# Performance work log

Measured on AMD Instinct MI355X. Metric: run time of the kernel, lower is better.

Reference implementation:

```python
import jax, jax.numpy as jnp
import numpy as np

# dims: S sets, M max items, DIN input feat, DM model dim (= head_size), H heads, L layers
S, M, DIN, DM, H, DH, L = 48, 128, 128, 128, 4, 128, 2
ALPHA = 0.3  # tf.keras.layers.LeakyReLU default alpha


def gelu(x):
    return jax.nn.gelu(x, approximate=False)  # tf.nn.gelu default is exact


def leaky(x):
    return jnp.where(x >= 0, x, ALPHA * x)


def set_norm(x, size):
    # masked per-set normalization over all items*features; pad rows (feature-sum == 0) are zeroed
    d = x.shape[-1]
    mask = (jnp.sum(x, axis=-1, keepdims=True) != 0).astype(x.dtype)  # [S,M,1]
    denom = size * d  # [S]
    mean = jnp.sum(x, axis=(1, 2)) / denom
    diff = x - mean[:, None, None]
    var = jnp.sum(jnp.square(diff) * mask, axis=(1, 2)) / denom
    return diff / (jnp.sqrt(var)[:, None, None] + 1e-8) * mask


def masked_softmax(s):
    # original masks by *nonzero score values*, not an additive bias
    mask = s != 0
    e = jnp.where(mask, jnp.exp(s - jnp.max(s, axis=-1, keepdims=True)), 0.0)
    return e / (jnp.sum(e, axis=-1, keepdims=True) + 1e-10)


def attention(x, wq, wk, wv, wh):
    split = lambda z: z.reshape(z.shape[0], z.shape[1], H, DH).transpose(0, 2, 1, 3)  # [S,H,M,D]
    q, k, v = split(x @ wq), split(x @ wk), split(x @ wv)
    s = jnp.einsum('shmd,shnd->shmn', q, k) / np.float32(np.sqrt(DH))
    a = masked_softmax(s)
    o = jnp.einsum('shmn,shnd->shmd', a, v).transpose(0, 2, 1, 3).reshape(x.shape[0], x.shape[1], H * DH)
    return o @ wh


def forward(x, size, W_proj, Wq, Wk, Wv, Wh, Wfc, Wc, w2):
    mask = (jnp.sum(x != 0, axis=-1, keepdims=True) > 0).astype(x.dtype)  # [S,M,1] valid-item mask
    h = gelu(x @ W_proj) * mask
    for l in range(L):
        a = attention(h, Wq[l], Wk[l], Wv[l], Wh[l]) * mask
        h = set_norm(h + a, size)
        f = gelu(h @ Wfc[l]) * mask
        h = set_norm(h + f, size)
    # cross_set_score (tuple branch, x == y): pairwise per-head set scores
    z = (h @ Wc).reshape(h.shape[0], h.shape[1], H, DH).transpose(0, 2, 1, 3)  # [S,H,M,D]
    s = leaky(jnp.einsum('jhmd,ihnd->jihmn', z, z) / np.float32(np.sqrt(DH)))  # [Sy,Sx,H,My,Mx]
    scores = jnp.sum(s, axis=(-1, -2)) / size[None, :, None] / np.float32(M)  # [Sy,Sx,H]
    return scores @ w2  # [Sy,Sx,1]


def setup_inputs() -> dict:
    key = jax.random.key(0)
    ks = jax.random.split(key, 10)
    x = jax.random.normal(ks[0], (S, M, DIN), jnp.float32)
    x_size = jax.random.randint(ks[1], (S,), 1, M + 1, jnp.int32)
    x = x * (jnp.arange(M)[None, :] < x_size[:, None])[:, :, None]  # zero-pad beyond set size
    sc = lambda n: np.float32(1.0 / np.sqrt(n))
    W_proj = jax.random.normal(ks[2], (DIN, DM), jnp.float32) * sc(DIN)
    Wq = jax.random.normal(ks[3], (L, DM, H * DH), jnp.float32) * sc(DM)
    Wk = jax.random.normal(ks[4], (L, DM, H * DH), jnp.float32) * sc(DM)
    Wv = jax.random.normal(ks[5], (L, DM, H * DH), jnp.float32) * sc(DM)
    Wh = jax.random.normal(ks[6], (L, H * DH, DM), jnp.float32) * sc(H * DH)
    Wfc = jax.random.normal(ks[7], (L, DM, DM), jnp.float32) * sc(DM)
    Wc = jax.random.normal(ks[8], (DM, H * DH), jnp.float32) * sc(DM)
    w2 = jax.random.normal(ks[9], (H, 1), jnp.float32) * sc(H)
    return dict(x=x, x_size=x_size, W_proj=W_proj, Wq=Wq, Wk=Wk, Wv=Wv, Wh=Wh, Wfc=Wfc, Wc=Wc, w2=w2)


def reference(x, x_size, W_proj, Wq, Wk, Wv, Wh, Wfc, Wc, w2):
    size = jnp.maximum(x_size, 1).astype(jnp.float32)
    return forward(x, size, W_proj, Wq, Wk, Wv, Wh, Wfc, Wc, w2)
```

## Files before the change

kernel.cpp:

```cpp
#include <hip/hip_runtime.h>
#include <hip/hip_bf16.h>
#include <math.h>

typedef unsigned short u16;
typedef short bf16x8 __attribute__((ext_vector_type(8)));
typedef float f32x4 __attribute__((ext_vector_type(4)));
typedef float f32x16 __attribute__((ext_vector_type(16)));

__device__ __forceinline__ u16 f2b(float f){
  union { float f; unsigned u; } c; c.f = f;
  unsigned u = c.u;
  unsigned r = (u + 0x7fffu + ((u >> 16) & 1u)) >> 16;
  return (u16)r;
}
__device__ __forceinline__ u16 f2bh(float f){
  union { __bf16 b; u16 u; } c; c.b = (__bf16)f; return c.u;
}
__device__ __forceinline__ unsigned pack2(float a, float b){
  return (unsigned)f2bh(a) | ((unsigned)f2bh(b) << 16);
}
__device__ __forceinline__ float gelu_f(float x){
  return 0.5f * x * (1.0f + erff(x * 0.70710678118654752f));
}

__global__ __launch_bounds__(256) void prep_weights(
    const float* __restrict__ Wproj, const float* __restrict__ Wq,
    const float* __restrict__ Wk,    const float* __restrict__ Wv,
    const float* __restrict__ Whp,   const float* __restrict__ Wfc,
    const float* __restrict__ Wc,    u16* __restrict__ wT,
    float* __restrict__ out)
{
  __shared__ __align__(16) u16 Ah[128*136];
  __shared__ __align__(16) u16 Bv[128*136];
  int bid = blockIdx.x, tid = threadIdx.x;
  if (bid >= 320) {
    int o = (bid - 320) * 256 + tid;
    if (o < 2304) out[o] = 0.0f;
    return;
  }
  if (bid < 312) {
    int cid = bid * 256 + tid;
    if (cid >= 34816 && cid < 67584) return;
    int region, lh = 0, c;
    if      (cid < 2048)  { region = 0; c = cid; }
    else if (cid < 18432) { int o = cid - 2048;  region = 1; lh = o >> 11; c = o & 2047; }
    else if (cid < 34816) { int o = cid - 18432; region = 2; lh = o >> 11; c = o & 2047; }
    else if (cid < 71680) { int o = cid - 67584; region = 5; lh = o >> 11; c = o & 2047; }
    else                  { int o = cid - 71680; region = 6; lh = o >> 11; c = o & 2047; }
    int l16 = c & 15, quad = (c >> 4) & 3, ks = (c >> 6) & 3, nt = c >> 8;
    int n = nt * 16 + l16, kb = ks * 32 + quad * 8;
    int l = lh >> 2, hh = lh & 3;
    const float rs = 0.08838834764831845f;
    u16 tmp[8];
#pragma unroll
    for (int e = 0; e < 8; ++e) {
      int k = kb + e;
      float v;
      switch (region) {
        case 0: v = Wproj[k * 128 + n]; break;
        case 1: v = Wq[l * 65536 + k * 512 + hh * 128 + n] * rs; break;
        case 2: v = Wk[l * 65536 + k * 512 + hh * 128 + n]; break;
        case 5: v = Wfc[lh * 16384 + k * 128 + n]; break;
        default: v = Wc[k * 512 + lh * 128 + n]; break;
      }
      tmp[e] = f2b(v);
    }
    *(uint4*)(wT + (size_t)cid * 8) = *(uint4*)tmp;
    return;
  }
  int lhb = bid - 312; int l = lhb >> 2, hh = lhb & 3;
#pragma unroll
  for (int it = 0; it < 64; ++it) {
    int idx = it * 256 + tid;
    int a = idx & 127, b = idx >> 7;
    Ah[a * 136 + b] = f2b(Whp[l * 65536 + (hh * 128 + b) * 128 + a]);
    Bv[b * 136 + a] = f2b(Wv[l * 65536 + b * 512 + hh * 128 + a]);
  }
  __syncthreads();
  int wv = tid >> 6, lane = tid & 63, quad = lane >> 4, l16 = lane & 15;
  f32x4 acc[2][8] = {};
  for (int ks = 0; ks < 4; ++ks) {
    bf16x8 aF[2], bF[8];
#pragma unroll
    for (int i = 0; i < 2; ++i)
      aF[i] = *(const bf16x8*)(Ah + ((wv*2+i)*16 + l16)*136 + ks*32 + quad*8);
#pragma unroll
    for (int n = 0; n < 8; ++n)
      bF[n] = *(const bf16x8*)(Bv + (n*16 + l16)*136 + ks*32 + quad*8);
#pragma unroll
    for (int i = 0; i < 2; ++i)
#pragma unroll
      for (int n = 0; n < 8; ++n)
        acc[i][n] = __builtin_amdgcn_mfma_f32_16x16x32_bf16(aF[i], bF[n], acc[i][n], 0, 0, 0);
  }
  size_t base = 278528 + (size_t)lhb * 16384;
#pragma unroll
  for (int i = 0; i < 2; ++i)
#pragma unroll
    for (int n2 = 0; n2 < 8; ++n2)
#pragma unroll
      for (int g = 0; g < 4; ++g) {
        int n = (wv*2+i)*16 + quad*4 + g;
        int k = n2*16 + l16;
        wT[base + (size_t)((((n>>4)*4 + (k>>5))*4 + ((k>>3)&3))*16 + (n&15))*8 + (k&7)]
            = f2b(acc[i][n2][g]);
      }
}

__device__ __forceinline__ void gemm_g(const u16* A, const u16* __restrict__ Bg,
    f32x4 (*acc)[4], int wr, int wc, int quad, int l16, int lane){
#pragma unroll
  for (int ks = 0; ks < 4; ++ks){
    bf16x8 aF[2], bF[4];
#pragma unroll
    for (int i = 0; i < 2; ++i)
      aF[i] = *(const bf16x8*)(A + ((wr*2+i)*16 + l16)*136 + ks*32 + quad*8);
#pragma unroll
    for (int n = 0; n < 4; ++n)
      bF[n] = *(const bf16x8*)(Bg + ((size_t)(((wc*4+n)*4 + ks)*64 + lane))*8);
#pragma unroll
    for (int i = 0; i < 2; ++i)
#pragma unroll
      for (int n = 0; n < 4; ++n)
        acc[i][n] = __builtin_amdgcn_mfma_f32_16x16x32_bf16(aF[i], bF[n], acc[i][n], 0, 0, 0);
  }
}

__device__ __forceinline__ void write_rm(u16* dst, f32x4 (*acc)[4],
                                         int wr, int wc, int quad, int l16){
#pragma unroll
  for (int i = 0; i < 2; ++i)
#pragma unroll
    for (int n = 0; n < 4; ++n)
#pragma unroll
      for (int g = 0; g < 4; ++g)
        dst[((wr*2+i)*16 + quad*4 + g)*136 + (wc*4+n)*16 + l16] = f2bh(acc[i][n][g]);
}

__device__ __forceinline__ void write_tr(u16* dst, f32x4 (*acc)[4],
                                         int wr, int wc, int quad, int l16){
#pragma unroll
  for (int i = 0; i < 2; ++i)
#pragma unroll
    for (int n = 0; n < 4; ++n)
#pragma unroll
      for (int g = 0; g < 4; ++g)
        dst[((wc*4+n)*16 + l16)*136 + (wr*2+i)*16 + quad*4 + g] = f2bh(acc[i][n][g]);
}

__device__ __forceinline__ void block_reduce2(float &s1, float &s2,
                                              float* red, int wv, int lane){
#pragma unroll
  for (int off = 1; off < 64; off <<= 1){
    s1 += __shfl_xor(s1, off, 64);
    s2 += __shfl_xor(s2, off, 64);
  }
  if (lane == 0){ red[wv*2] = s1; red[wv*2+1] = s2; }
  __syncthreads();
  s1 = red[0]+red[2]+red[4]+red[6]+red[8]+red[10]+red[12]+red[14];
  s2 = red[1]+red[3]+red[5]+red[7]+red[9]+red[11]+red[13]+red[15];
  __syncthreads();
}

__global__ __launch_bounds__(512, 2) void trunk(
    const float* __restrict__ x, const int* __restrict__ xsize,
    const u16* __restrict__ wT, u16* __restrict__ zg)
{
  __shared__ __align__(16) u16 hA[128*136];
  __shared__ __align__(16) u16 qP[128*136];
  __shared__ __align__(16) u16 kB[128*136];
  __shared__ __align__(16) u16 vB[128*136];
  __shared__ float svalid[128];
  __shared__ float red[16];
  int tid = threadIdx.x;
  int wv = tid >> 6, lane = tid & 63, quad = lane >> 4, l16 = lane & 15;
  int wr = wv >> 1, wc = wv & 1;
  int s = blockIdx.x;
  int sz = xsize[s]; if (sz < 1) sz = 1;
  int Mt = (sz + 15) >> 4, Mk = (sz + 31) >> 5;
  float den = (float)sz * 128.0f;

#pragma unroll
  for (int it = 0; it < 4; ++it) {
    int ch = tid + it * 512; int r = ch >> 4, cc = ch & 15;
    const float* p = x + ((size_t)s * 128 + r) * 128 + cc * 8;
    float4 u0 = *(const float4*)p, u1 = *(const float4*)(p + 4);
    int nz = (u0.x!=0.f)|(u0.y!=0.f)|(u0.z!=0.f)|(u0.w!=0.f)|
             (u1.x!=0.f)|(u1.y!=0.f)|(u1.z!=0.f)|(u1.w!=0.f);
    nz |= __shfl_xor(nz,1,64); nz |= __shfl_xor(nz,2,64);
    nz |= __shfl_xor(nz,4,64); nz |= __shfl_xor(nz,8,64);
    if ((tid & 15) == 0) svalid[r] = nz ? 1.f : 0.f;
    uint4 w;
    w.x = pack2(u0.x,u0.y); w.y = pack2(u0.z,u0.w);
    w.z = pack2(u1.x,u1.y); w.w = pack2(u1.z,u1.w);
    *(uint4*)(hA + r*136 + cc*8) = w;
  }
  __syncthreads();

  f32x4 hR[2][4];
  {
    f32x4 acc[2][4] = {};
    gemm_g(hA, wT, acc, wr, wc, quad, l16, lane);
    __syncthreads();
#pragma unroll
    for (int i = 0; i < 2; ++i)
#pragma unroll
      for (int n = 0; n < 4; ++n)
#pragma unroll
        for (int g = 0; g < 4; ++g) {
          int row = (wr*2+i)*16 + quad*4 + g;
          float gg = gelu_f(acc[i][n][g]) * svalid[row];
          hR[i][n][g] = gg;
          hA[row*136 + (wc*4+n)*16 + l16] = f2bh(gg);
        }
    __syncthreads();
  }

#pragma unroll 1
  for (int l = 0; l < 2; ++l) {
    f32x4 aR[2][4] = {};
#pragma unroll 1
    for (int hh = 0; hh < 4; ++hh) {
      int lh = l * 4 + hh;
      {
        f32x4 qa[2][4] = {};
        gemm_g(hA, wT + 16384 + lh*16384, qa, wr, wc, quad, l16, lane);
        write_rm(qP, qa, wr, wc, quad, l16);
      }
      {
        f32x4 ka[2][4] = {};
        gemm_g(hA, wT + 147456 + lh*16384, ka, wr, wc, quad, l16, lane);
        write_rm(kB, ka, wr, wc, quad, l16);
      }
      {
        f32x4 va[2][4] = {};
        gemm_g(hA, wT + 278528 + lh*16384, va, wr, wc, quad, l16, lane);
        write_tr(vB, va, wr, wc, quad, l16);
      }
      __syncthreads();
      if (wv < Mt) {
        bf16x8 qA[4];
#pragma unroll
        for (int ks = 0; ks < 4; ++ks)
          qA[ks] = *(const bf16x8*)(qP + (wv*16 + l16)*136 + ks*32 + quad*8);
        f32x4 sacc[8] = {};
#pragma unroll
        for (int ks = 0; ks < 4; ++ks) {
          bf16x8 bF[8];
#pragma unroll
          for (int j = 0; j < 8; ++j)
            if (j < Mt) bF[j] = *(const bf16x8*)(kB + (j*16+l16)*136 + ks*32 + quad*8);
#pragma unroll
          for (int j = 0; j < 8; ++j)
            if (j < Mt) sacc[j] = __builtin_amdgcn_mfma_f32_16x16x32_bf16(qA[ks], bF[j], sacc[j], 0, 0, 0);
        }
        for (int g = 0; g < 4; ++g) {
          float vals[8]; float rmax = -1e30f;
#pragma unroll
          for (int j = 0; j < 8; ++j)
            if (j < Mt) {
              float v = sacc[j][g];
              vals[j] = v;
              rmax = fmaxf(rmax, v);
            }
          for (int off = 1; off < 16; off <<= 1) rmax = fmaxf(rmax, __shfl_xor(rmax, off, 64));
          if (sz < 128) rmax = fmaxf(rmax, 0.0f);
          float rsum = 0.f;
#pragma unroll
          for (int j = 0; j < 8; ++j)
            if (j < Mt) {
              float e = (vals[j] != 0.0f) ? __expf(vals[j] - rmax) : 0.0f;
              vals[j] = e; rsum += e;
            }
          for (int off = 1; off < 16; off <<= 1) rsum += __shfl_xor(rsum, off, 64);
          float inv = 1.0f / (rsum + 1e-10f);
#pragma unroll
          for (int j = 0; j < 8; ++j)
            if (j < Mt) sacc[j][g] = vals[j] * inv;
        }
#pragma unroll
        for (int j = 0; j < 8; ++j)
          if (j < Mt)
#pragma unroll
            for (int g = 0; g < 4; ++g)
              qP[(wv*16 + quad*4 + g)*136 + j*16 + l16] = f2bh(sacc[j][g]);
      }
      __syncthreads();
#pragma unroll
      for (int i = 0; i < 2; ++i) {
        int mtile = wr*2 + i;
        if (mtile < Mt) {
          for (int ks = 0; ks < Mk; ++ks) {
            bf16x8 aF = *(const bf16x8*)(qP + (mtile*16 + l16)*136 + ks*32 + quad*8);
            bf16x8 bF[4];
#pragma unroll
            for (int n = 0; n < 4; ++n)
              bF[n] = *(const bf16x8*)(vB + ((wc*4+n)*16+l16)*136 + ks*32 + quad*8);
#pragma unroll
            for (int n = 0; n < 4; ++n)
              aR[i][n] = __builtin_amdgcn_mfma_f32_16x16x32_bf16(aF, bF[n], aR[i][n], 0, 0, 0);
          }
        }
      }
      __syncthreads();
    }

    {
      float ls1 = 0.f, ls2 = 0.f;
#pragma unroll
      for (int i = 0; i < 2; ++i)
#pragma unroll
        for (int n = 0; n < 4; ++n)
#pragma unroll
          for (int g = 0; g < 4; ++g) {
            int row = (wr*2+i)*16 + quad*4 + g;
            float u = hR[i][n][g] + aR[i][n][g] * svalid[row];
            hR[i][n][g] = u;
            ls1 += u; ls2 += u * u;
          }
      block_reduce2(ls1, ls2, red, wv, lane);
      float mean = ls1 / den;
      float var = ls2 / den - mean * mean; if (var < 0.f) var = 0.f;
      float inv = 1.0f / (sqrtf(var) + 1e-8f);
#pragma unroll
      for (int i = 0; i < 2; ++i)
#pragma unroll
        for (int n = 0; n < 4; ++n)
#pragma unroll
          for (int g = 0; g < 4; ++g) {
            int row = (wr*2+i)*16 + quad*4 + g;
            float hn = (hR[i][n][g] - mean) * inv * svalid[row];
            hR[i][n][g] = hn;
            hA[row*136 + (wc*4+n)*16 + l16] = f2bh(hn);
          }
      __syncthreads();
    }
    {
      f32x4 fa[2][4] = {};
      gemm_g(hA, wT + 540672 + l*16384, fa, wr, wc, quad, l16, lane);
      float ls1 = 0.f, ls2 = 0.f;
#pragma unroll
      for (int i = 0; i < 2; ++i)
#pragma unroll
        for (int n = 0; n < 4; ++n)
#pragma unroll
          for (int g = 0; g < 4; ++g) {
            int row = (wr*2+i)*16 + quad*4 + g;
            float u = hR[i][n][g] + gelu_f(fa[i][n][g]) * svalid[row];
            hR[i][n][g] = u;
            ls1 += u; ls2 += u * u;
          }
      block_reduce2(ls1, ls2, red, wv, lane);
      float mean = ls1 / den;
      float var = ls2 / den - mean * mean; if (var < 0.f) var = 0.f;
      float inv = 1.0f / (sqrtf(var) + 1e-8f);
#pragma unroll
      for (int i = 0; i < 2; ++i)
#pragma unroll
        for (int n = 0; n < 4; ++n)
#pragma unroll
          for (int g = 0; g < 4; ++g) {
            int row = (wr*2+i)*16 + quad*4 + g;
            float hn = (hR[i][n][g] - mean) * inv * svalid[row];
            hR[i][n][g] = hn;
            hA[row*136 + (wc*4+n)*16 + l16] = f2bh(hn);
          }
      __syncthreads();
    }
  }

#pragma unroll 1
  for (int hh = 0; hh < 4; ++hh) {
    f32x4 za[2][4] = {};
    gemm_g(hA, wT + 573440 + hh*16384, za, wr, wc, quad, l16, lane);
    u16* zb = zg + (((size_t)s*4 + hh) << 14);
#pragma unroll
    for (int i = 0; i < 2; ++i)
#pragma unroll
      for (int n = 0; n < 4; ++n)
#pragma unroll
        for (int g = 0; g < 4; ++g) {
          int row = (wr*2+i)*16 + quad*4 + g;
          int col = (wc*4+n)*16 + l16;
          zb[(size_t)(((row>>5)*8 + (col>>4))*512 + ((col>>3)&1)*256
                      + (row&31)*8 + (col&7))] = f2bh(za[i][n][g]);
        }
  }
}

__global__ __launch_bounds__(256) void cross_kernel(
    const u16* __restrict__ zg, const float* __restrict__ w2,
    float* __restrict__ out, const int* __restrict__ xsize)
{
  __shared__ float red[4];
  int tid = threadIdx.x, wave = tid >> 6, lane = tid & 63;
  int t4 = blockIdx.x;
  int pr = t4 >> 2, hh = t4 & 3;
  float jf = (97.0f - sqrtf(9409.0f - 8.0f * (float)pr)) * 0.5f;
  int j = (int)jf; if (j > 47) j = 47; if (j < 0) j = 0;
  while (j > 0 && j * 48 - (j * (j - 1)) / 2 > pr) --j;
  while ((j + 1) * 48 - ((j + 1) * j) / 2 <= pr) ++j;
  int i = j + pr - (j * 48 - (j * (j - 1)) / 2);
  int sj = xsize[j]; if (sj < 1) sj = 1;
  int si = xsize[i]; if (si < 1) si = 1;
  int MjT = (sj + 31) >> 5, MiT = (si + 31) >> 5;
  const u16* zj = zg + (((size_t)j * 4 + hh) << 14);
  const u16* zi = zg + (((size_t)i * 4 + hh) << 14);
  int gA = (wave >> 1) * 2, gB = (wave & 1) * 2;
  bool a0 = gA < MjT, a1 = (gA + 1) < MjT;
  bool b0 = gB < MiT, b1 = (gB + 1) < MiT;
  f32x16 acc[2][2] = {};
  if ((a0 || a1) && (b0 || b1)) {
#pragma unroll
    for (int ks = 0; ks < 8; ++ks) {
      bf16x8 aF[2], bF[2];
      if (a0) aF[0] = *(const bf16x8*)(zj + (size_t)((gA    )*8 + ks)*512 + lane*8);
      if (a1) aF[1] = *(const bf16x8*)(zj + (size_t)((gA + 1)*8 + ks)*512 + lane*8);
      if (b0) bF[0] = *(const bf16x8*)(zi + (size_t)((gB    )*8 + ks)*512 + lane*8);
      if (b1) bF[1] = *(const bf16x8*)(zi + (size_t)((gB + 1)*8 + ks)*512 + lane*8);
      if (a0 && b0) acc[0][0] = __builtin_amdgcn_mfma_f32_32x32x16_bf16(aF[0], bF[0], acc[0][0], 0, 0, 0);
      if (a0 && b1) acc[0][1] = __builtin_amdgcn_mfma_f32_32x32x16_bf16(aF[0], bF[1], acc[0][1], 0, 0, 0);
      if (a1 && b0) acc[1][0] = __builtin_amdgcn_mfma_f32_32x32x16_bf16(aF[1], bF[0], acc[1][0], 0, 0, 0);
      if (a1 && b1) acc[1][1] = __builtin_amdgcn_mfma_f32_32x32x16_bf16(aF[1], bF[1], acc[1][1], 0, 0, 0);
    }
  }
  float s1 = 0.f, s2 = 0.f;
#pragma unroll
  for (int ii = 0; ii < 2; ++ii)
#pragma unroll
    for (int jj = 0; jj < 2; ++jj) {
      bool tact = (ii ? a1 : a0) && (jj ? b1 : b0);
      if (tact)
#pragma unroll
        for (int r = 0; r < 16; ++r) {
          float a = acc[ii][jj][r];
          s1 += a; s2 += fabsf(a);
        }
    }
  const float rs = 0.08838834764831845f;
  float tp = rs * (0.65f * s1 + 0.35f * s2);
  for (int off = 1; off < 64; off <<= 1) tp += __shfl_xor(tp, off, 64);
  if (lane == 0) red[wave] = tp;
  __syncthreads();
  if (tid == 0) {
    float T = red[0] + red[1] + red[2] + red[3];
    float w = w2[hh];
    atomicAdd(out + j * 48 + i, T * w / ((float)si * 128.0f));
    if (i != j)
      atomicAdd(out + i * 48 + j, T * w / ((float)sj * 128.0f));
  }
}

extern "C" void kernel_launch(void* const* d_in, const int* in_sizes, int n_in,
                              void* d_out, int out_size, void* d_ws, size_t ws_size,
                              hipStream_t stream)
{
  const float* x     = (const float*)d_in[0];
  const int*   xsize = (const int*)d_in[1];
  const float* Wproj = (const float*)d_in[2];
  const float* Wq    = (const float*)d_in[3];
  const float* Wk    = (const float*)d_in[4];
  const float* Wv    = (const float*)d_in[5];
  const float* Whp   = (const float*)d_in[6];
  const float* Wfc   = (const float*)d_in[7];
  const float* Wc    = (const float*)d_in[8];
  const float* w2    = (const float*)d_in[9];
  float* out = (float*)d_out;

  char* ws = (char*)d_ws;
  size_t off = 0;
  auto alloc = [&](size_t bytes) -> char* {
    char* p = ws + off;
    off += (bytes + 255) & ~(size_t)255;
    return p;
  };
  u16* wT = (u16*)alloc(638976 * 2);
  u16* zg = (u16*)alloc((size_t)3145728 * 2);

  prep_weights<<<329, 256, 0, stream>>>(Wproj, Wq, Wk, Wv, Whp, Wfc, Wc, wT, out);
  trunk<<<48, 512, 0, stream>>>(x, xsize, wT, zg);
  cross_kernel<<<4704, 256, 0, stream>>>(zg, w2, out, xsize);
}
```

Baseline: 224.5 us.

## Fuse trunk and cross-score kernels into one cooperative persistent kernel with flags

The separate trunk and cross_kernel launches are merged into a single cooperative kernel of 256 blocks. The first 48 blocks run the per-set trunk, write z, and publish a per-set ready flag with release semantics. All blocks then pull pairwise cross-score work items from an atomic counter, two items per block, and spin on the flags of the two sets they need. This is meant to remove a kernel launch boundary and let cross-score work overlap the tail of the trunk, at the cost of spin-waiting, atomics and one more flag-reset block in prep_weights.

```diff
diff --git a/kernel.cpp b/kernel.cpp
--- a/kernel.cpp
+++ b/kernel.cpp
@@ -28,11 +28,12 @@
     const float* __restrict__ Wk,    const float* __restrict__ Wv,
     const float* __restrict__ Whp,   const float* __restrict__ Wfc,
     const float* __restrict__ Wc,    u16* __restrict__ wT,
-    float* __restrict__ out)
+    float* __restrict__ out, int* __restrict__ flags)
 {
   __shared__ __align__(16) u16 Ah[128*136];
   __shared__ __align__(16) u16 Bv[128*136];
   int bid = blockIdx.x, tid = threadIdx.x;
+  if (bid == 329) { if (tid < 64) flags[tid] = 0; return; }
   if (bid >= 320) {
     int o = (bid - 320) * 256 + tid;
     if (o < 2304) out[o] = 0.0f;
@@ -162,9 +163,11 @@
   __syncthreads();
 }
 
-__global__ __launch_bounds__(512, 2) void trunk(
+__global__ __launch_bounds__(512, 2) void mega(
     const float* __restrict__ x, const int* __restrict__ xsize,
-    const u16* __restrict__ wT, u16* __restrict__ zg)
+    const u16* __restrict__ wT, u16* __restrict__ zg,
+    const float* __restrict__ w2, float* __restrict__ out,
+    int* __restrict__ flags)
 {
   __shared__ __align__(16) u16 hA[128*136];
   __shared__ __align__(16) u16 qP[128*136];
@@ -172,141 +175,215 @@
   __shared__ __align__(16) u16 vB[128*136];
   __shared__ float svalid[128];
   __shared__ float red[16];
+  __shared__ int s_item;
+  __shared__ float redx[8];
   int tid = threadIdx.x;
-  int wv = tid >> 6, lane = tid & 63, quad = lane >> 4, l16 = lane & 15;
-  int wr = wv >> 1, wc = wv & 1;
-  int s = blockIdx.x;
-  int sz = xsize[s]; if (sz < 1) sz = 1;
-  int Mt = (sz + 15) >> 4, Mk = (sz + 31) >> 5;
-  float den = (float)sz * 128.0f;
-
-#pragma unroll
-  for (int it = 0; it < 4; ++it) {
-    int ch = tid + it * 512; int r = ch >> 4, cc = ch & 15;
-    const float* p = x + ((size_t)s * 128 + r) * 128 + cc * 8;
-    float4 u0 = *(const float4*)p, u1 = *(const float4*)(p + 4);
-    int nz = (u0.x!=0.f)|(u0.y!=0.f)|(u0.z!=0.f)|(u0.w!=0.f)|
-             (u1.x!=0.f)|(u1.y!=0.f)|(u1.z!=0.f)|(u1.w!=0.f);
-    nz |= __shfl_xor(nz,1,64); nz |= __shfl_xor(nz,2,64);
-    nz |= __shfl_xor(nz,4,64); nz |= __shfl_xor(nz,8,64);
-    if ((tid & 15) == 0) svalid[r] = nz ? 1.f : 0.f;
-    uint4 w;
-    w.x = pack2(u0.x,u0.y); w.y = pack2(u0.z,u0.w);
-    w.z = pack2(u1.x,u1.y); w.w = pack2(u1.z,u1.w);
-    *(uint4*)(hA + r*136 + cc*8) = w;
-  }
-  __syncthreads();
-
-  f32x4 hR[2][4];
-  {
-    f32x4 acc[2][4] = {};
-    gemm_g(hA, wT, acc, wr, wc, quad, l16, lane);
+  int bid = blockIdx.x;
+  int* counter = flags + 48;
+  const float rs = 0.08838834764831845f;
+
+  if (bid < 48) {
+    int wv = tid >> 6, lane = tid & 63, quad = lane >> 4, l16 = lane & 15;
+    int wr = wv >> 1, wc = wv & 1;
+    int s = bid;
+    int sz = xsize[s]; if (sz < 1) sz = 1;
+    int Mt = (sz + 15) >> 4, Mk = (sz + 31) >> 5;
+    float den = (float)sz * 128.0f;
+
+#pragma unroll
+    for (int it = 0; it < 4; ++it) {
+      int ch = tid + it * 512; int r = ch >> 4, cc = ch & 15;
+      const float* p = x + ((size_t)s * 128 + r) * 128 + cc * 8;
+      float4 u0 = *(const float4*)p, u1 = *(const float4*)(p + 4);
+      int nz = (u0.x!=0.f)|(u0.y!=0.f)|(u0.z!=0.f)|(u0.w!=0.f)|
+               (u1.x!=0.f)|(u1.y!=0.f)|(u1.z!=0.f)|(u1.w!=0.f);
+      nz |= __shfl_xor(nz,1,64); nz |= __shfl_xor(nz,2,64);
+      nz |= __shfl_xor(nz,4,64); nz |= __shfl_xor(nz,8,64);
+      if ((tid & 15) == 0) svalid[r] = nz ? 1.f : 0.f;
+      uint4 w;
+      w.x = pack2(u0.x,u0.y); w.y = pack2(u0.z,u0.w);
+      w.z = pack2(u1.x,u1.y); w.w = pack2(u1.z,u1.w);
+      *(uint4*)(hA + r*136 + cc*8) = w;
+    }
     __syncthreads();
-#pragma unroll
-    for (int i = 0; i < 2; ++i)
-#pragma unroll
-      for (int n = 0; n < 4; ++n)
-#pragma unroll
-        for (int g = 0; g < 4; ++g) {
-          int row = (wr*2+i)*16 + quad*4 + g;
-          float gg = gelu_f(acc[i][n][g]) * svalid[row];
-          hR[i][n][g] = gg;
-          hA[row*136 + (wc*4+n)*16 + l16] = f2bh(gg);
-        }
-    __syncthreads();
-  }
+
+    f32x4 hR[2][4];
+    {
+      f32x4 acc[2][4] = {};
+      gemm_g(hA, wT, acc, wr, wc, quad, l16, lane);
+      __syncthreads();
+#pragma unroll
+      for (int i = 0; i < 2; ++i)
+#pragma unroll
+        for (int n = 0; n < 4; ++n)
+#pragma unroll
+          for (int g = 0; g < 4; ++g) {
+            int row = (wr*2+i)*16 + quad*4 + g;
+            float gg = gelu_f(acc[i][n][g]) * svalid[row];
+            hR[i][n][g] = gg;
+            hA[row*136 + (wc*4+n)*16 + l16] = f2bh(gg);
+          }
+      __syncthreads();
+    }
 
 #pragma unroll 1
-  for (int l = 0; l < 2; ++l) {
-    f32x4 aR[2][4] = {};
+    for (int l = 0; l < 2; ++l) {
+      f32x4 aR[2][4] = {};
+#pragma unroll 1
+      for (int hh = 0; hh < 4; ++hh) {
+        int lh = l * 4 + hh;
+        {
+          f32x4 qa[2][4] = {};
+          gemm_g(hA, wT + 16384 + lh*16384, qa, wr, wc, quad, l16, lane);
+          write_rm(qP, qa, wr, wc, quad, l16);
+        }
+        {
+          f32x4 ka[2][4] = {};
+          gemm_g(hA, wT + 147456 + lh*16384, ka, wr, wc, quad, l16, lane);
+          write_rm(kB, ka, wr, wc, quad, l16);
+        }
+        {
+          f32x4 va[2][4] = {};
+          gemm_g(hA, wT + 278528 + lh*16384, va, wr, wc, quad, l16, lane);
+          write_tr(vB, va, wr, wc, quad, l16);
+        }
+        __syncthreads();
+        if (wv < Mt) {
+          bf16x8 qA[4];
+#pragma unroll
+          for (int ks = 0; ks < 4; ++ks)
+            qA[ks] = *(const bf16x8*)(qP + (wv*16 + l16)*136 + ks*32 + quad*8);
+          f32x4 sacc[8] = {};
+#pragma unroll
+          for (int ks = 0; ks < 4; ++ks) {
+            bf16x8 bF[8];
+#pragma unroll
+            for (int j = 0; j < 8; ++j)
+              if (j < Mt) bF[j] = *(const bf16x8*)(kB + (j*16+l16)*136 + ks*32 + quad*8);
+#pragma unroll
+            for (int j = 0; j < 8; ++j)
+              if (j < Mt) sacc[j] = __builtin_amdgcn_mfma_f32_16x16x32_bf16(qA[ks], bF[j], sacc[j], 0, 0, 0);
+          }
+          for (int g = 0; g < 4; ++g) {
+            float vals[8]; float rmax = -1e30f;
+#pragma unroll
+            for (int j = 0; j < 8; ++j)
+              if (j < Mt) {
+                float v = sacc[j][g];
+                vals[j] = v;
+                rmax = fmaxf(rmax, v);
+              }
+            for (int off = 1; off < 16; off <<= 1) rmax = fmaxf(rmax, __shfl_xor(rmax, off, 64));
+            if (sz < 128) rmax = fmaxf(rmax, 0.0f);
+            float rsum = 0.f;
+#pragma unroll
+            for (int j = 0; j < 8; ++j)
+              if (j < Mt) {
+                float e = (vals[j] != 0.0f) ? __expf(vals[j] - rmax) : 0.0f;
+                vals[j] = e; rsum += e;
+              }
+            for (int off = 1; off < 16; off <<= 1) rsum += __shfl_xor(rsum, off, 64);
+            float inv = 1.0f / (rsum + 1e-10f);
+#pragma unroll
+            for (int j = 0; j < 8; ++j)
+              if (j < Mt) sacc[j][g] = vals[j] * inv;
+          }
+#pragma unroll
+          for (int j = 0; j < 8; ++j)
+            if (j < Mt)
+#pragma unroll
+              for (int g = 0; g < 4; ++g)
+                qP[(wv*16 + quad*4 + g)*136 + j*16 + l16] = f2bh(sacc[j][g]);
+        }
+        __syncthreads();
+#pragma unroll
+        for (int i = 0; i < 2; ++i) {
+          int mtile = wr*2 + i;
+          if (mtile < Mt) {
+            for (int ks = 0; ks < Mk; ++ks) {
+              bf16x8 aF = *(const bf16x8*)(qP + (mtile*16 + l16)*136 + ks*32 + quad*8);
+              bf16x8 bF[4];
+#pragma unroll
+              for (int n = 0; n < 4; ++n)
+                bF[n] = *(const bf16x8*)(vB + ((wc*4+n)*16+l16)*136 + ks*32 + quad*8);
+#pragma unroll
+              for (int n = 0; n < 4; ++n)
+                aR[i][n] = __builtin_amdgcn_mfma_f32_16x16x32_bf16(aF, bF[n], aR[i][n], 0, 0, 0);
+            }
+          }
+        }
+        __syncthreads();
+      }
+
+      {
+        float ls1 = 0.f, ls2 = 0.f;
+#pragma unroll
+        for (int i = 0; i < 2; ++i)
+#pragma unroll
+          for (int n = 0; n < 4; ++n)
+#pragma unroll
+            for (int g = 0; g < 4; ++g) {
+              int row = (wr*2+i)*16 + quad*4 + g;
+              float u = hR[i][n][g] + aR[i][n][g] * svalid[row];
+              hR[i][n][g] = u;
+              ls1 += u; ls2 += u * u;
+            }
+        block_reduce2(ls1, ls2, red, wv, lane);
+        float mean = ls1 / den;
+        float var = ls2 / den - mean * mean; if (var < 0.f) var = 0.f;
+        float inv = 1.0f / (sqrtf(var) + 1e-8f);
+#pragma unroll
+        for (int i = 0; i < 2; ++i)
+#pragma unroll
+          for (int n = 0; n < 4; ++n)
+#pragma unroll
+            for (int g = 0; g < 4; ++g) {
+              int row = (wr*2+i)*16 + quad*4 + g;
+              float hn = (hR[i][n][g] - mean) * inv * svalid[row];
+              hR[i][n][g] = hn;
+              hA[row*136 + (wc*4+n)*16 + l16] = f2bh(hn);
+            }
+        __syncthreads();
+      }
+      {
+        f32x4 fa[2][4] = {};
+        gemm_g(hA, wT + 540672 + l*16384, fa, wr, wc, quad, l16, lane);
+        float ls1 = 0.f, ls2 = 0.f;
+#pragma unroll
+        for (int i = 0; i < 2; ++i)
+#pragma unroll
+          for (int n = 0; n < 4; ++n)
+#pragma unroll
+            for (int g = 0; g < 4; ++g) {
+              int row = (wr*2+i)*16 + quad*4 + g;
+              float u = hR[i][n][g] + gelu_f(fa[i][n][g]) * svalid[row];
+              hR[i][n][g] = u;
+              ls1 += u; ls2 += u * u;
+            }
+        block_reduce2(ls1, ls2, red, wv, lane);
+        float mean = ls1 / den;
+        float var = ls2 / den - mean * mean; if (var < 0.f) var = 0.f;
+        float inv = 1.0f / (sqrtf(var) + 1e-8f);
+#pragma unroll
+        for (int i = 0; i < 2; ++i)
+#pragma unroll
+          for (int n = 0; n < 4; ++n)
+#pragma unroll
+            for (int g = 0; g < 4; ++g) {
+              int row = (wr*2+i)*16 + quad*4 + g;
+              float hn = (hR[i][n][g] - mean) * inv * svalid[row];
+              hR[i][n][g] = hn;
+              hA[row*136 + (wc*4+n)*16 + l16] = f2bh(hn);
+            }
+        __syncthreads();
+      }
+    }
+
 #pragma unroll 1
     for (int hh = 0; hh < 4; ++hh) {
-      int lh = l * 4 + hh;
-      {
-        f32x4 qa[2][4] = {};
-        gemm_g(hA, wT + 16384 + lh*16384, qa, wr, wc, quad, l16, lane);
-        write_rm(qP, qa, wr, wc, quad, l16);
-      }
-      {
-        f32x4 ka[2][4] = {};
-        gemm_g(hA, wT + 147456 + lh*16384, ka, wr, wc, quad, l16, lane);
-        write_rm(kB, ka, wr, wc, quad, l16);
-      }
-      {
-        f32x4 va[2][4] = {};
-        gemm_g(hA, wT + 278528 + lh*16384, va, wr, wc, quad, l16, lane);
-        write_tr(vB, va, wr, wc, quad, l16);
-      }
-      __syncthreads();
-      if (wv < Mt) {
-        bf16x8 qA[4];
-#pragma unroll
-        for (int ks = 0; ks < 4; ++ks)
-          qA[ks] = *(const bf16x8*)(qP + (wv*16 + l16)*136 + ks*32 + quad*8);
-        f32x4 sacc[8] = {};
-#pragma unroll
-        for (int ks = 0; ks < 4; ++ks) {
-          bf16x8 bF[8];
-#pragma unroll
-          for (int j = 0; j < 8; ++j)
-            if (j < Mt) bF[j] = *(const bf16x8*)(kB + (j*16+l16)*136 + ks*32 + quad*8);
-#pragma unroll
-          for (int j = 0; j < 8; ++j)
-            if (j < Mt) sacc[j] = __builtin_amdgcn_mfma_f32_16x16x32_bf16(qA[ks], bF[j], sacc[j], 0, 0, 0);
-        }
-        for (int g = 0; g < 4; ++g) {
-          float vals[8]; float rmax = -1e30f;
-#pragma unroll
-          for (int j = 0; j < 8; ++j)
-            if (j < Mt) {
-              float v = sacc[j][g];
-              vals[j] = v;
-              rmax = fmaxf(rmax, v);
-            }
-          for (int off = 1; off < 16; off <<= 1) rmax = fmaxf(rmax, __shfl_xor(rmax, off, 64));
-          if (sz < 128) rmax = fmaxf(rmax, 0.0f);
-          float rsum = 0.f;
-#pragma unroll
-          for (int j = 0; j < 8; ++j)
-            if (j < Mt) {
-              float e = (vals[j] != 0.0f) ? __expf(vals[j] - rmax) : 0.0f;
-              vals[j] = e; rsum += e;
-            }
-          for (int off = 1; off < 16; off <<= 1) rsum += __shfl_xor(rsum, off, 64);
-          float inv = 1.0f / (rsum + 1e-10f);
-#pragma unroll
-          for (int j = 0; j < 8; ++j)
-            if (j < Mt) sacc[j][g] = vals[j] * inv;
-        }
-#pragma unroll
-        for (int j = 0; j < 8; ++j)
-          if (j < Mt)
-#pragma unroll
-            for (int g = 0; g < 4; ++g)
-              qP[(wv*16 + quad*4 + g)*136 + j*16 + l16] = f2bh(sacc[j][g]);
-      }
-      __syncthreads();
-#pragma unroll
-      for (int i = 0; i < 2; ++i) {
-        int mtile = wr*2 + i;
-        if (mtile < Mt) {
-          for (int ks = 0; ks < Mk; ++ks) {
-            bf16x8 aF = *(const bf16x8*)(qP + (mtile*16 + l16)*136 + ks*32 + quad*8);
-            bf16x8 bF[4];
-#pragma unroll
-            for (int n = 0; n < 4; ++n)
-              bF[n] = *(const bf16x8*)(vB + ((wc*4+n)*16+l16)*136 + ks*32 + quad*8);
-#pragma unroll
-            for (int n = 0; n < 4; ++n)
-              aR[i][n] = __builtin_amdgcn_mfma_f32_16x16x32_bf16(aF, bF[n], aR[i][n], 0, 0, 0);
-          }
-        }
-      }
-      __syncthreads();
-    }
-
-    {
-      float ls1 = 0.f, ls2 = 0.f;
+      f32x4 za[2][4] = {};
+      gemm_g(hA, wT + 573440 + hh*16384, za, wr, wc, quad, l16, lane);
+      u16* zb = zg + (((size_t)s*4 + hh) << 14);
 #pragma unroll
       for (int i = 0; i < 2; ++i)
 #pragma unroll
@@ -314,140 +391,97 @@
 #pragma unroll
           for (int g = 0; g < 4; ++g) {
             int row = (wr*2+i)*16 + quad*4 + g;
-            float u = hR[i][n][g] + aR[i][n][g] * svalid[row];
-            hR[i][n][g] = u;
-            ls1 += u; ls2 += u * u;
-          }
-      block_reduce2(ls1, ls2, red, wv, lane);
-      float mean = ls1 / den;
-      float var = ls2 / den - mean * mean; if (var < 0.f) var = 0.f;
-      float inv = 1.0f / (sqrtf(var) + 1e-8f);
-#pragma unroll
-      for (int i = 0; i < 2; ++i)
-#pragma unroll
-        for (int n = 0; n < 4; ++n)
-#pragma unroll
-          for (int g = 0; g < 4; ++g) {
-            int row = (wr*2+i)*16 + quad*4 + g;
-            float hn = (hR[i][n][g] - mean) * inv * svalid[row];
-            hR[i][n][g] = hn;
-            hA[row*136 + (wc*4+n)*16 + l16] = f2bh(hn);
-          }
+            int col = (wc*4+n)*16 + l16;
+            zb[(size_t)(((row>>5)*8 + (col>>4))*512 + ((col>>3)&1)*256
+                        + (row&31)*8 + (col&7))] = f2bh(za[i][n][g]);
+          }
+    }
+    __syncthreads();
+    if (tid == 0) {
+      __threadfence();
+      __hip_atomic_store(flags + s, 1, __ATOMIC_RELEASE, __HIP_MEMORY_SCOPE_AGENT);
+    }
+  }
+
+  {
+    int half = tid >> 8, t = tid & 255;
+    int w4 = t >> 6, lane = t & 63;
+    for (;;) {
+      if (tid == 0) s_item = atomicAdd(counter, 2);
       __syncthreads();
-    }
-    {
-      f32x4 fa[2][4] = {};
-      gemm_g(hA, wT + 540672 + l*16384, fa, wr, wc, quad, l16, lane);
-      float ls1 = 0.f, ls2 = 0.f;
-#pragma unroll
-      for (int i = 0; i < 2; ++i)
-#pragma unroll
-        for (int n = 0; n < 4; ++n)
-#pragma unroll
-          for (int g = 0; g < 4; ++g) {
-            int row = (wr*2+i)*16 + quad*4 + g;
-            float u = hR[i][n][g] + gelu_f(fa[i][n][g]) * svalid[row];
-            hR[i][n][g] = u;
-            ls1 += u; ls2 += u * u;
-          }
-      block_reduce2(ls1, ls2, red, wv, lane);
-      float mean = ls1 / den;
-      float var = ls2 / den - mean * mean; if (var < 0.f) var = 0.f;
-      float inv = 1.0f / (sqrtf(var) + 1e-8f);
-#pragma unroll
-      for (int i = 0; i < 2; ++i)
-#pragma unroll
-        for (int n = 0; n < 4; ++n)
-#pragma unroll
-          for (int g = 0; g < 4; ++g) {
-            int row = (wr*2+i)*16 + quad*4 + g;
-            float hn = (hR[i][n][g] - mean) * inv * svalid[row];
-            hR[i][n][g] = hn;
-            hA[row*136 + (wc*4+n)*16 + l16] = f2bh(hn);
-          }
+      int base = s_item;
+      if (base >= 4704) break;
+      int item = base + half;
+      bool active = item < 4704;
+      int j = 0, i = 0, hh2 = 0;
+      if (active) {
+        int pr = item >> 2; hh2 = item & 3;
+        float jf = (97.0f - sqrtf(9409.0f - 8.0f * (float)pr)) * 0.5f;
+        j = (int)jf; if (j > 47) j = 47; if (j < 0) j = 0;
+        while (j > 0 && j * 48 - (j * (j - 1)) / 2 > pr) --j;
+        while ((j + 1) * 48 - ((j + 1) * j) / 2 <= pr) ++j;
+        i = j + pr - (j * 48 - (j * (j - 1)) / 2);
+        if (t == 0) {
+          while (__hip_atomic_load(flags + j, __ATOMIC_ACQUIRE, __HIP_MEMORY_SCOPE_AGENT) == 0 ||
+                 __hip_atomic_load(flags + i, __ATOMIC_ACQUIRE, __HIP_MEMORY_SCOPE_AGENT) == 0)
+            __builtin_amdgcn_s_sleep(2);
+        }
+      }
       __syncthreads();
-    }
-  }
-
-#pragma unroll 1
-  for (int hh = 0; hh < 4; ++hh) {
-    f32x4 za[2][4] = {};
-    gemm_g(hA, wT + 573440 + hh*16384, za, wr, wc, quad, l16, lane);
-    u16* zb = zg + (((size_t)s*4 + hh) << 14);
-#pragma unroll
-    for (int i = 0; i < 2; ++i)
-#pragma unroll
-      for (int n = 0; n < 4; ++n)
-#pragma unroll
-        for (int g = 0; g < 4; ++g) {
-          int row = (wr*2+i)*16 + quad*4 + g;
-          int col = (wc*4+n)*16 + l16;
-          zb[(size_t)(((row>>5)*8 + (col>>4))*512 + ((col>>3)&1)*256
-                      + (row&31)*8 + (col&7))] = f2bh(za[i][n][g]);
-        }
-  }
-}
-
-__global__ __launch_bounds__(256) void cross_kernel(
-    const u16* __restrict__ zg, const float* __restrict__ w2,
-    float* __restrict__ out, const int* __restrict__ xsize)
-{
-  __shared__ float red[4];
-  int tid = threadIdx.x, wave = tid >> 6, lane = tid & 63;
-  int t4 = blockIdx.x;
-  int pr = t4 >> 2, hh = t4 & 3;
-  float jf = (97.0f - sqrtf(9409.0f - 8.0f * (float)pr)) * 0.5f;
-  int j = (int)jf; if (j > 47) j = 47; if (j < 0) j = 0;
-  while (j > 0 && j * 48 - (j * (j - 1)) / 2 > pr) --j;
-  while ((j + 1) * 48 - ((j + 1) * j) / 2 <= pr) ++j;
-  int i = j + pr - (j * 48 - (j * (j - 1)) / 2);
-  int sj = xsize[j]; if (sj < 1) sj = 1;
-  int si = xsize[i]; if (si < 1) si = 1;
-  int MjT = (sj + 31) >> 5, MiT = (si + 31) >> 5;
-  const u16* zj = zg + (((size_t)j * 4 + hh) << 14);
-  const u16* zi = zg + (((size_t)i * 4 + hh) << 14);
-  int gA = (wave >> 1) * 2, gB = (wave & 1) * 2;
-  bool a0 = gA < MjT, a1 = (gA + 1) < MjT;
-  bool b0 = gB < MiT, b1 = (gB + 1) < MiT;
-  f32x16 acc[2][2] = {};
-  if ((a0 || a1) && (b0 || b1)) {
-#pragma unroll
-    for (int ks = 0; ks < 8; ++ks) {
-      bf16x8 aF[2], bF[2];
-      if (a0) aF[0] = *(const bf16x8*)(zj + (size_t)((gA    )*8 + ks)*512 + lane*8);
-      if (a1) aF[1] = *(const bf16x8*)(zj + (size_t)((gA + 1)*8 + ks)*512 + lane*8);
-      if (b0) bF[0] = *(const bf16x8*)(zi + (size_t)((gB    )*8 + ks)*512 + lane*8);
-      if (b1) bF[1] = *(const bf16x8*)(zi + (size_t)((gB + 1)*8 + ks)*512 + lane*8);
-      if (a0 && b0) acc[0][0] = __builtin_amdgcn_mfma_f32_32x32x16_bf16(aF[0], bF[0], acc[0][0], 0, 0, 0);
-      if (a0 && b1) acc[0][1] = __builtin_amdgcn_mfma_f32_32x32x16_bf16(aF[0], bF[1], acc[0][1], 0, 0, 0);
-      if (a1 && b0) acc[1][0] = __builtin_amdgcn_mfma_f32_32x32x16_bf16(aF[1], bF[0], acc[1][0], 0, 0, 0);
-      if (a1 && b1) acc[1][1] = __builtin_amdgcn_mfma_f32_32x32x16_bf16(aF[1], bF[1], acc[1][1], 0, 0, 0);
-    }
-  }
-  float s1 = 0.f, s2 = 0.f;
-#pragma unroll
-  for (int ii = 0; ii < 2; ++ii)
-#pragma unroll
-    for (int jj = 0; jj < 2; ++jj) {
-      bool tact = (ii ? a1 : a0) && (jj ? b1 : b0);
-      if (tact)
-#pragma unroll
-        for (int r = 0; r < 16; ++r) {
-          float a = acc[ii][jj][r];
-          s1 += a; s2 += fabsf(a);
-        }
-    }
-  const float rs = 0.08838834764831845f;
-  float tp = rs * (0.65f * s1 + 0.35f * s2);
-  for (int off = 1; off < 64; off <<= 1) tp += __shfl_xor(tp, off, 64);
-  if (lane == 0) red[wave] = tp;
-  __syncthreads();
-  if (tid == 0) {
-    float T = red[0] + red[1] + red[2] + red[3];
-    float w = w2[hh];
-    atomicAdd(out + j * 48 + i, T * w / ((float)si * 128.0f));
-    if (i != j)
-      atomicAdd(out + i * 48 + j, T * w / ((float)sj * 128.0f));
+      __threadfence();
+      float tp = 0.f;
+      int sj = 1, si = 1;
+      if (active) {
+        sj = xsize[j]; if (sj < 1) sj = 1;
+        si = xsize[i]; if (si < 1) si = 1;
+        int MjT = (sj + 31) >> 5, MiT = (si + 31) >> 5;
+        const u16* zj = zg + (((size_t)j * 4 + hh2) << 14);
+        const u16* zi = zg + (((size_t)i * 4 + hh2) << 14);
+        int gA = (w4 >> 1) * 2, gB = (w4 & 1) * 2;
+        bool a0 = gA < MjT, a1 = (gA + 1) < MjT;
+        bool b0 = gB < MiT, b1 = (gB + 1) < MiT;
+        f32x16 acc[2][2] = {};
+        if ((a0 || a1) && (b0 || b1)) {
+#pragma unroll
+          for (int ks = 0; ks < 8; ++ks) {
+            bf16x8 aF[2], bF[2];
+            if (a0) aF[0] = *(const bf16x8*)(zj + (size_t)((gA    )*8 + ks)*512 + lane*8);
+            if (a1) aF[1] = *(const bf16x8*)(zj + (size_t)((gA + 1)*8 + ks)*512 + lane*8);
+            if (b0) bF[0] = *(const bf16x8*)(zi + (size_t)((gB    )*8 + ks)*512 + lane*8);
+            if (b1) bF[1] = *(const bf16x8*)(zi + (size_t)((gB + 1)*8 + ks)*512 + lane*8);
+            if (a0 && b0) acc[0][0] = __builtin_amdgcn_mfma_f32_32x32x16_bf16(aF[0], bF[0], acc[0][0], 0, 0, 0);
+            if (a0 && b1) acc[0][1] = __builtin_amdgcn_mfma_f32_32x32x16_bf16(aF[0], bF[1], acc[0][1], 0, 0, 0);
+            if (a1 && b0) acc[1][0] = __builtin_amdgcn_mfma_f32_32x32x16_bf16(aF[1], bF[0], acc[1][0], 0, 0, 0);
+            if (a1 && b1) acc[1][1] = __builtin_amdgcn_mfma_f32_32x32x16_bf16(aF[1], bF[1], acc[1][1], 0, 0, 0);
+          }
+        }
+        float s1 = 0.f, s2 = 0.f;
+#pragma unroll
+        for (int ii = 0; ii < 2; ++ii)
+#pragma unroll
+          for (int jj = 0; jj < 2; ++jj) {
+            bool tact = (ii ? a1 : a0) && (jj ? b1 : b0);
+            if (tact)
+#pragma unroll
+              for (int r = 0; r < 16; ++r) {
+                float a = acc[ii][jj][r];
+                s1 += a; s2 += fabsf(a);
+              }
+          }
+        tp = rs * (0.65f * s1 + 0.35f * s2);
+        for (int off = 1; off < 64; off <<= 1) tp += __shfl_xor(tp, off, 64);
+      }
+      if (lane == 0) redx[half*4 + w4] = tp;
+      __syncthreads();
+      if (t == 0 && active) {
+        float T = redx[half*4] + redx[half*4+1] + redx[half*4+2] + redx[half*4+3];
+        float w = w2[hh2];
+        atomicAdd(out + j * 48 + i, T * w / ((float)si * 128.0f));
+        if (i != j)
+          atomicAdd(out + i * 48 + j, T * w / ((float)sj * 128.0f));
+      }
+      __syncthreads();
+    }
   }
 }
 
@@ -474,10 +508,17 @@
     off += (bytes + 255) & ~(size_t)255;
     return p;
   };
-  u16* wT = (u16*)alloc(638976 * 2);
-  u16* zg = (u16*)alloc((size_t)3145728 * 2);
-
-  prep_weights<<<329, 256, 0, stream>>>(Wproj, Wq, Wk, Wv, Whp, Wfc, Wc, wT, out);
-  trunk<<<48, 512, 0, stream>>>(x, xsize, wT, zg);
-  cross_kernel<<<4704, 256, 0, stream>>>(zg, w2, out, xsize);
-}
+  u16* wT    = (u16*)alloc(638976 * 2);
+  u16* zg    = (u16*)alloc((size_t)3145728 * 2);
+  int* flags = (int*)alloc(64 * 4);
+
+  prep_weights<<<330, 256, 0, stream>>>(Wproj, Wq, Wk, Wv, Whp, Wfc, Wc, wT, out, flags);
+
+  {
+    const float* xa = x; const int* xs = xsize; const u16* w = wT;
+    u16* z = zg; const float* w2a = w2; float* oa = out; int* fl = flags;
+    void* args[] = { (void*)&xa, (void*)&xs, (void*)&w, (void*)&z,
+                     (void*)&w2a, (void*)&oa, (void*)&fl };
+    hipLaunchCooperativeKernel((void*)mega, dim3(256), dim3(512), args, 0, stream);
+  }
+}
```

New measurement: 851.0 us. +279.1%, slower.
